# Kernel optimization log

Measured on AMD Instinct MI355X. Metric: run time of the kernel, lower is better.

## Reference

```python
import jax, jax.numpy as jnp
import numpy as np

BINS = 10

def setup_inputs() -> dict:
    key = jax.random.key(0)
    k1, k2 = jax.random.split(key)
    N, C = 262144, 512
    x = jax.random.normal(k1, (N, C), dtype=jnp.float32)
    target = jax.random.randint(k2, (N,), 0, C, dtype=jnp.int64)
    return {"x": x, "target": target}

def reference(x, target):
    # log-softmax + NLL (reduction='none', no class weights)
    log_p = jax.nn.log_softmax(x, axis=-1)                      # [N, C]
    log_pt = jnp.take_along_axis(log_p, target[:, None].astype(jnp.int32), axis=1)[:, 0]  # [N]
    ce = -log_pt                                                # NLL per-sample
    # gradient-norm proxy g = |pt - 1|, detached
    g = jax.lax.stop_gradient(jnp.abs(jnp.exp(log_pt) - 1.0))   # [N]
    bin_idx = jnp.floor(g * (BINS - 0.0001)).astype(jnp.int32)  # [N] in [0, BINS)
    # histogram (first call: _last_bin_count is None -> raw counts, no EMA)
    bin_count = jnp.zeros((BINS,), dtype=x.dtype).at[bin_idx].add(1.0)
    nonempty = jnp.sum(bin_count > 0).astype(x.dtype)
    gd = jnp.maximum(bin_count * nonempty, 0.0001)
    beta = 1.0 / gd                                             # [BINS]
    loss = jax.lax.stop_gradient(beta[bin_idx]) * ce            # [N]
    return loss.mean()                                          # reduction='mean'
```

## Files before the change

kernel.cpp:

```cpp
#include <hip/hip_runtime.h>
#include <hip/hip_bf16.h>

#define BINS 10
#define C 512
#define NBLK 2048


__device__ __forceinline__ void process_row(const float4 (&v)[8], float xt,
                                            int sub,
                                            float* s_cnt, float* s_sum) {
    float s = 0.0f;
    #pragma unroll
    for (int j = 0; j < 8; ++j)
        s += __expf(v[j].x) + __expf(v[j].y) + __expf(v[j].z) + __expf(v[j].w);
    #pragma unroll
    for (int off = 8; off >= 1; off >>= 1)
        s += __shfl_xor(s, off);
    float lse = __logf(s);
    float ce  = lse - xt;
    float pt  = __expf(xt - lse);
    float g   = fabsf(pt - 1.0f);
    int   bin = (int)(g * (BINS - 0.0001f));
    bin = bin < 0 ? 0 : (bin > BINS - 1 ? BINS - 1 : bin);
    if (sub == 0) {
        atomicAdd(&s_cnt[bin], 1.0f);
        atomicAdd(&s_sum[bin], ce);
    }
}

__global__ __launch_bounds__(256, 2) void ghmc_pass1(const float* __restrict__ x,
                                                     const int* __restrict__ target,
                                                     float* __restrict__ slots,
                                                     int N) {
    __shared__ float s_cnt[BINS];
    __shared__ float s_sum[BINS];
    const int tid = threadIdx.x;
    if (tid < BINS) { s_cnt[tid] = 0.0f; s_sum[tid] = 0.0f; }
    __syncthreads();

    const int sub    = tid & 15;
    const int grp    = tid >> 4;
    const int row0   = blockIdx.x * 16 + grp;
    const int stride = gridDim.x * 16;

    float4 a[8];
    float  xtA = 0.0f;
    if (row0 < N) {
        const float4* rp = (const float4*)(x + (size_t)row0 * C);
        int t = target[row0];
        #pragma unroll
        for (int j = 0; j < 8; ++j) a[j] = rp[sub + 16 * j];
        xtA = x[(size_t)row0 * C + t];
    }

    for (int row = row0; row < N; row += 2 * stride) {
        const int rowB = row + stride;
        const bool hasB = rowB < N;

        float4 b[8];
        float  xtB = 0.0f;
        if (hasB) {
            const float4* rp = (const float4*)(x + (size_t)rowB * C);
            int t = target[rowB];
            #pragma unroll
            for (int j = 0; j < 8; ++j) b[j] = rp[sub + 16 * j];
            xtB = x[(size_t)rowB * C + t];
        }

        process_row(a, xtA, sub, s_cnt, s_sum);

        const int rowN2 = row + 2 * stride;
        if (rowN2 < N) {
            const float4* rp = (const float4*)(x + (size_t)rowN2 * C);
            int t = target[rowN2];
            #pragma unroll
            for (int j = 0; j < 8; ++j) a[j] = rp[sub + 16 * j];
            xtA = x[(size_t)rowN2 * C + t];
        }

        if (hasB)
            process_row(b, xtB, sub, s_cnt, s_sum);
    }

    __syncthreads();
    if (tid < BINS) {
        slots[blockIdx.x * 2 * BINS + tid]        = s_cnt[tid];
        slots[blockIdx.x * 2 * BINS + BINS + tid] = s_sum[tid];
    }
}

__global__ __launch_bounds__(256) void ghmc_pass2(const float* __restrict__ slots,
                                                  float* __restrict__ out,
                                                  int nblk, float invN) {
    __shared__ float red[256][2 * BINS];
    const int tid = threadIdx.x;

    float c[2 * BINS];
    #pragma unroll
    for (int k = 0; k < 2 * BINS; ++k) c[k] = 0.0f;

    for (int b = tid; b < nblk; b += 256) {
        const float* sp = slots + (size_t)b * 2 * BINS;
        #pragma unroll
        for (int k = 0; k < 2 * BINS; ++k) c[k] += sp[k];
    }
    #pragma unroll
    for (int k = 0; k < 2 * BINS; ++k) red[tid][k] = c[k];
    __syncthreads();

    for (int off = 128; off >= 1; off >>= 1) {
        if (tid < off) {
            #pragma unroll
            for (int k = 0; k < 2 * BINS; ++k)
                red[tid][k] += red[tid + off][k];
        }
        __syncthreads();
    }

    if (tid == 0) {
        int ne = 0;
        #pragma unroll
        for (int b = 0; b < BINS; ++b)
            if (red[0][b] > 0.0f) ne++;
        float nef = (float)ne;
        float acc = 0.0f;
        #pragma unroll
        for (int b = 0; b < BINS; ++b) {
            float gd = fmaxf(red[0][b] * nef, 0.0001f);
            acc += red[0][BINS + b] / gd;
        }
        out[0] = acc * invN;
    }
}

extern "C" void kernel_launch(void* const* d_in, const int* in_sizes, int n_in,
                              void* d_out, int out_size, void* d_ws, size_t ws_size,
                              hipStream_t stream) {
    const float* x      = (const float*)d_in[0];
    const int*   target = (const int*)d_in[1];
    float*       out    = (float*)d_out;
    float*       slots  = (float*)d_ws;

    const int N = in_sizes[1];

    int nblk = NBLK;
    size_t need = (size_t)nblk * 2 * BINS * sizeof(float);
    if (ws_size < need) {
        nblk = (int)(ws_size / (2 * BINS * sizeof(float)));
        if (nblk < 1) nblk = 1;
    }

    ghmc_pass1<<<nblk, 256, 0, stream>>>(x, target, slots, N);
    ghmc_pass2<<<1, 256, 0, stream>>>(slots, out, nblk, 1.0f / (float)N);
}
```

Before: 98.79 us.

## Transpose partial-sum slots to bin-major and reduce with per-wave shuffles

Pass 1 now writes per-block partial counts and sums in bin-major order so pass 2 reads each bin column contiguously. Pass 2 gives each of its four waves five columns, reduces them with wave shuffles, and drops the shared-memory tree reduction and its repeated barriers. The pass-1 grid shrinks from 2048 to 512 blocks, which cuts partial-sum traffic but leaves fewer blocks to hide memory latency in the main streaming pass.

```diff
diff --git a/kernel.cpp b/kernel.cpp
--- a/kernel.cpp
+++ b/kernel.cpp
@@ -3,7 +3,7 @@
 
 #define BINS 10
 #define C 512
-#define NBLK 2048
+#define NBLK 512
 
 
 __device__ __forceinline__ void process_row(const float4 (&v)[8], float xt,
@@ -31,7 +31,7 @@
 __global__ __launch_bounds__(256, 2) void ghmc_pass1(const float* __restrict__ x,
                                                      const int* __restrict__ target,
                                                      float* __restrict__ slots,
-                                                     int N) {
+                                                     int N, int nblk) {
     __shared__ float s_cnt[BINS];
     __shared__ float s_sum[BINS];
     const int tid = threadIdx.x;
@@ -84,50 +84,41 @@
 
     __syncthreads();
     if (tid < BINS) {
-        slots[blockIdx.x * 2 * BINS + tid]        = s_cnt[tid];
-        slots[blockIdx.x * 2 * BINS + BINS + tid] = s_sum[tid];
+        slots[(size_t)tid * nblk + blockIdx.x]          = s_cnt[tid];
+        slots[(size_t)(BINS + tid) * nblk + blockIdx.x] = s_sum[tid];
     }
 }
 
 __global__ __launch_bounds__(256) void ghmc_pass2(const float* __restrict__ slots,
                                                   float* __restrict__ out,
                                                   int nblk, float invN) {
-    __shared__ float red[256][2 * BINS];
-    const int tid = threadIdx.x;
+    __shared__ float red[2 * BINS];
+    const int tid  = threadIdx.x;
+    const int lane = tid & 63;
+    const int wave = tid >> 6;
 
-    float c[2 * BINS];
-    #pragma unroll
-    for (int k = 0; k < 2 * BINS; ++k) c[k] = 0.0f;
-
-    for (int b = tid; b < nblk; b += 256) {
-        const float* sp = slots + (size_t)b * 2 * BINS;
+    for (int k = wave * 5; k < wave * 5 + 5; ++k) {
+        const float* col = slots + (size_t)k * nblk;
+        float s = 0.0f;
+        for (int j = lane; j < nblk; j += 64) s += col[j];
         #pragma unroll
-        for (int k = 0; k < 2 * BINS; ++k) c[k] += sp[k];
+        for (int off = 32; off >= 1; off >>= 1)
+            s += __shfl_xor(s, off);
+        if (lane == 0) red[k] = s;
     }
-    #pragma unroll
-    for (int k = 0; k < 2 * BINS; ++k) red[tid][k] = c[k];
     __syncthreads();
-
-    for (int off = 128; off >= 1; off >>= 1) {
-        if (tid < off) {
-            #pragma unroll
-            for (int k = 0; k < 2 * BINS; ++k)
-                red[tid][k] += red[tid + off][k];
-        }
-        __syncthreads();
-    }
 
     if (tid == 0) {
         int ne = 0;
         #pragma unroll
         for (int b = 0; b < BINS; ++b)
-            if (red[0][b] > 0.0f) ne++;
+            if (red[b] > 0.0f) ne++;
         float nef = (float)ne;
         float acc = 0.0f;
         #pragma unroll
         for (int b = 0; b < BINS; ++b) {
-            float gd = fmaxf(red[0][b] * nef, 0.0001f);
-            acc += red[0][BINS + b] / gd;
+            float gd = fmaxf(red[b] * nef, 0.0001f);
+            acc += red[BINS + b] / gd;
         }
         out[0] = acc * invN;
     }
@@ -150,6 +141,6 @@
         if (nblk < 1) nblk = 1;
     }
 
-    ghmc_pass1<<<nblk, 256, 0, stream>>>(x, target, slots, N);
+    ghmc_pass1<<<nblk, 256, 0, stream>>>(x, target, slots, N, nblk);
     ghmc_pass2<<<1, 256, 0, stream>>>(slots, out, nblk, 1.0f / (float)N);
 }
```

After: 107.1 us. +8.4%, slower.
